# Kernel optimization log

Hardware: AMD Instinct MI355X
Metric: run time of the kernel (lower is better)

## Reference

```python
import jax, jax.numpy as jnp
import numpy as np

EPS = 1e-5
NUM_GROUPS = 32
HT_MIN = -2.0
HT_MAX = 2.0


def setup_inputs() -> dict:
    key = jax.random.key(0)
    k1, k2 = jax.random.split(key)
    B, Cin, Cout, H, W = 32, 256, 512, 56, 56
    x = jax.random.normal(k1, (B, Cin, H, W), dtype=jnp.float32)
    weight = jax.random.normal(k2, (Cout, Cin), dtype=jnp.float32)
    gamma = jnp.ones((Cout,), dtype=jnp.float32)
    beta = jnp.zeros((Cout,), dtype=jnp.float32)
    return {"x": x, "weight": weight, "gamma": gamma, "beta": beta}


def reference(x, weight, gamma, beta) -> jnp.ndarray:
    B, Cin, H, W = x.shape
    Cout = weight.shape[0]
    G = NUM_GROUPS
    # 1x1-conv style GEMM over channels (no bias in the original kernel call)
    y = jnp.einsum("oc,bchw->bohw", weight, x)  # [B, Cout, H, W]
    # GroupNorm: stats over (channels-in-group, H, W) per sample
    yg = y.reshape(B, G, Cout // G, H, W)
    mean = jnp.mean(yg, axis=(2, 3, 4), keepdims=True)
    var = jnp.var(yg, axis=(2, 3, 4), keepdims=True)
    yn = ((yg - mean) * jax.lax.rsqrt(var + EPS)).reshape(B, Cout, H, W)
    yn = yn * gamma[None, :, None, None] + beta[None, :, None, None]
    # HardTanh clamp
    return jnp.clip(yn, HT_MIN, HT_MAX)
```

## Files before the change

kernel.cpp:

```cpp
#include <hip/hip_runtime.h>


#define HW    3136
#define CIN   256
#define COUT  512
#define BATCH 32
#define NG    32
#define CPG   16
#define EPS   1e-5f

typedef _Float16 f16x8 __attribute__((ext_vector_type(8)));
typedef float    f32x4 __attribute__((ext_vector_type(4)));
typedef unsigned int u32;

__device__ __forceinline__ void gload16(const void* g, void* l) {
  __builtin_amdgcn_global_load_lds(
      (const u32 __attribute__((address_space(1)))*)g,
      (u32 __attribute__((address_space(3)))*)l, 16, 0, 0);
}

__global__ __launch_bounds__(256) void k0_transpose(
    const float* __restrict__ x, const float* __restrict__ w,
    _Float16* __restrict__ xT, _Float16* __restrict__ wf)
{
  __shared__ float T[64 * 65];
  const int bid = blockIdx.x;
  const int t   = threadIdx.x;
  const int b   = bid / 196;
  const int r   = bid % 196;
  const int st  = r >> 2;
  const int ct  = r & 3;
  const int s0  = st * 64, c0 = ct * 64;

  const float* xb = x + ((size_t)b * CIN + c0) * HW + s0;
#pragma unroll
  for (int rr = 0; rr < 4; ++rr) {
    const int c_loc = (t >> 4) + rr * 16;
    const int s4    = (t & 15) * 4;
    const float4 v  = *(const float4*)(xb + (size_t)c_loc * HW + s4);
    T[(s4 + 0) * 65 + c_loc] = v.x;
    T[(s4 + 1) * 65 + c_loc] = v.y;
    T[(s4 + 2) * 65 + c_loc] = v.z;
    T[(s4 + 3) * 65 + c_loc] = v.w;
  }
  __syncthreads();
#pragma unroll
  for (int p = 0; p < 2; ++p) {
    const int s_loc = p * 32 + (t >> 3);
    const int cg    = (t & 7) * 8;
    f16x8 o;
#pragma unroll
    for (int j = 0; j < 8; ++j) o[j] = (_Float16)T[s_loc * 65 + cg + j];
    *(f16x8*)(xT + ((size_t)b * HW + s0 + s_loc) * CIN + c0 + cg) = o;
  }
  if (bid < (COUT * CIN) / 256) wf[bid * 256 + t] = (_Float16)w[bid * 256 + t];
}

__global__ __launch_bounds__(256) void k_gemm(
    const _Float16* __restrict__ xT, const _Float16* __restrict__ wf,
    float2* __restrict__ stats, _Float16* __restrict__ y)
{
  __shared__ __align__(16) _Float16 As[2 * 128 * 32];
  __shared__ __align__(16) _Float16 Bs[2 * 128 * 32];

  const int bid  = blockIdx.x;
  const int tile = (bid & 7) * 400 + (bid >> 3);
  const int mt   = tile & 3;
  const int q2   = tile >> 2;
  const int nt   = q2 % 25;
  const int b    = q2 / 25;
  const int s0   = (nt == 24) ? (HW - 128) : nt * 128;

  const int t    = threadIdx.x;
  const int lane = t & 63;
  const int wid  = t >> 6;
  const int wy   = wid >> 1, wx = wid & 1;

  const int r_st = t >> 2;
  const int ch   = (t & 3) ^ ((r_st >> 1) & 3);

  const _Float16* xb = xT + (size_t)b * HW * CIN;
  const _Float16* gA0 = wf + (size_t)(mt * 128 + r_st) * CIN + ch * 8;
  const _Float16* gA1 = gA0 + (size_t)64 * CIN;
  const _Float16* gB0 = xb + (size_t)(s0 + r_st) * CIN + ch * 8;
  const _Float16* gB1 = gB0 + (size_t)64 * CIN;

  f32x4 acc[4][4] = {};

#define STAGE(bufi, kt_)                                                  \
  do {                                                                    \
    gload16(gA0 + (kt_) * 32, As + (bufi) * 4096 + t * 8);                \
    gload16(gA1 + (kt_) * 32, As + (bufi) * 4096 + 2048 + t * 8);         \
    gload16(gB0 + (kt_) * 32, Bs + (bufi) * 4096 + t * 8);                \
    gload16(gB1 + (kt_) * 32, Bs + (bufi) * 4096 + 2048 + t * 8);         \
  } while (0)

  STAGE(0, 0);
  __syncthreads();

  const int c = lane >> 4;
#pragma unroll
  for (int kt = 0; kt < 8; ++kt) {
    const int cur = kt & 1;
    if (kt < 7) STAGE(cur ^ 1, kt + 1);

    f16x8 af[4], bfr[4];
#pragma unroll
    for (int mi = 0; mi < 4; ++mi) {
      const int m = wy * 64 + mi * 16 + (lane & 15);
      af[mi] = *(const f16x8*)(As + cur * 4096 + m * 32 +
                               ((c ^ ((m >> 1) & 3)) * 8));
    }
#pragma unroll
    for (int ni = 0; ni < 4; ++ni) {
      const int n = wx * 64 + ni * 16 + (lane & 15);
      bfr[ni] = *(const f16x8*)(Bs + cur * 4096 + n * 32 +
                                ((c ^ ((n >> 1) & 3)) * 8));
    }
#pragma unroll
    for (int mi = 0; mi < 4; ++mi)
#pragma unroll
      for (int ni = 0; ni < 4; ++ni)
        acc[mi][ni] = __builtin_amdgcn_mfma_f32_16x16x32_f16(
            af[mi], bfr[ni], acc[mi][ni], 0, 0, 0);

    __syncthreads();
  }
#undef STAGE

  const int slo  = (nt == 24) ? 3072 : 0;
  const int colb = s0 + wx * 64 + (lane & 15);
#pragma unroll
  for (int mi = 0; mi < 4; ++mi) {
    float s1 = 0.f, s2 = 0.f;
#pragma unroll
    for (int ni = 0; ni < 4; ++ni) {
      if (colb + ni * 16 >= slo) {
#pragma unroll
        for (int rr = 0; rr < 4; ++rr) {
          const float v = acc[mi][ni][rr];
          s1 += v; s2 += v * v;
        }
      }
    }
#pragma unroll
    for (int off = 32; off > 0; off >>= 1) {
      s1 += __shfl_down(s1, off, 64);
      s2 += __shfl_down(s2, off, 64);
    }
    if (lane == 0) {
      const int g = mt * 8 + wy * 4 + mi;
      stats[((b * NG + g) * 25 + nt) * 2 + wx] = make_float2(s1, s2);
    }
    const int row0 = mt * 128 + wy * 64 + mi * 16 + ((lane >> 4) << 2);
#pragma unroll
    for (int rr = 0; rr < 4; ++rr) {
      _Float16* yrow = y + ((size_t)b * COUT + row0 + rr) * HW + colb;
#pragma unroll
      for (int ni = 0; ni < 4; ++ni)
        if (colb + ni * 16 >= slo) yrow[ni * 16] = (_Float16)acc[mi][ni][rr];
    }
  }
}

__global__ __launch_bounds__(256) void k_finalize(
    const float2* __restrict__ stats, const float* __restrict__ gamma,
    const float* __restrict__ beta, float* __restrict__ ss)
{
  const int i = blockIdx.x * 256 + threadIdx.x;
  if (i < BATCH * COUT) {
    const int b  = i >> 9;
    const int co = i & (COUT - 1);
    const int g  = co >> 4;
    const float2* sp = stats + (size_t)(b * NG + g) * 50;
    float s1 = 0.f, s2 = 0.f;
#pragma unroll 10
    for (int j = 0; j < 50; ++j) { s1 += sp[j].x; s2 += sp[j].y; }
    const float cnt  = (float)(CPG * HW);
    const float mean = s1 / cnt;
    const float var  = s2 / cnt - mean * mean;
    const float rsig = rsqrtf(var + EPS);
    const float sc   = rsig * gamma[co];
    ss[i * 2 + 0] = sc;
    ss[i * 2 + 1] = beta[co] - mean * sc;
  }
}

__global__ __launch_bounds__(256) void k_norm(
    const _Float16* __restrict__ y, const float* __restrict__ ss,
    float* __restrict__ out)
{
  const u32 u   = blockIdx.x * 256 + threadIdx.x;
  const u32 row = u / (HW / 8);
  const u32 sp  = (u - row * (HW / 8)) * 8;
  const float sc = ss[row * 2 + 0];
  const float sh = ss[row * 2 + 1];
  const f16x8 v = *(const f16x8*)(y + (size_t)row * HW + sp);
  f32x4 o0, o1;
  o0[0] = fminf(fmaxf((float)v[0] * sc + sh, -2.0f), 2.0f);
  o0[1] = fminf(fmaxf((float)v[1] * sc + sh, -2.0f), 2.0f);
  o0[2] = fminf(fmaxf((float)v[2] * sc + sh, -2.0f), 2.0f);
  o0[3] = fminf(fmaxf((float)v[3] * sc + sh, -2.0f), 2.0f);
  o1[0] = fminf(fmaxf((float)v[4] * sc + sh, -2.0f), 2.0f);
  o1[1] = fminf(fmaxf((float)v[5] * sc + sh, -2.0f), 2.0f);
  o1[2] = fminf(fmaxf((float)v[6] * sc + sh, -2.0f), 2.0f);
  o1[3] = fminf(fmaxf((float)v[7] * sc + sh, -2.0f), 2.0f);
  float* op = out + (size_t)row * HW + sp;
  __builtin_nontemporal_store(o0, (f32x4*)(op));
  __builtin_nontemporal_store(o1, (f32x4*)(op + 4));
}

extern "C" void kernel_launch(void* const* d_in, const int* in_sizes, int n_in,
                              void* d_out, int out_size, void* d_ws, size_t ws_size,
                              hipStream_t stream)
{
  const float* x     = (const float*)d_in[0];
  const float* w     = (const float*)d_in[1];
  const float* gamma = (const float*)d_in[2];
  const float* beta  = (const float*)d_in[3];
  float* out = (float*)d_out;

  const size_t xT_bytes = (size_t)BATCH * HW * CIN * 2;
  const size_t wf_bytes = (size_t)COUT * CIN * 2;
  const size_t st_bytes = (size_t)BATCH * NG * 50 * 8;
  const size_t ss_bytes = (size_t)BATCH * COUT * 2 * 4;
  const size_t y_bytes  = (size_t)BATCH * COUT * HW * 2;

  char* ws = (char*)d_ws;
  _Float16* xT = (_Float16*)ws;
  _Float16* wf = (_Float16*)(ws + xT_bytes);
  float2* stats = (float2*)(ws + xT_bytes + wf_bytes);
  float* ss    = (float*)(ws + xT_bytes + wf_bytes + st_bytes);
  _Float16* y  = (_Float16*)(ws + xT_bytes + wf_bytes + st_bytes + ss_bytes);

  if (ws_size < xT_bytes + wf_bytes + st_bytes + ss_bytes + y_bytes) return;

  k0_transpose<<<dim3(BATCH * 196), dim3(256), 0, stream>>>(x, w, xT, wf);
  k_gemm<<<dim3(BATCH * 100), dim3(256), 0, stream>>>(xT, wf, stats, y);
  k_finalize<<<dim3(BATCH * COUT / 256), dim3(256), 0, stream>>>(stats, gamma, beta, ss);
  k_norm<<<dim3(BATCH * COUT * HW / 8 / 256), dim3(256), 0, stream>>>(y, ss, out);
}
```

Measured before the change: 377.9 us.

## Recompute GEMM in a second pass to fuse normalization and drop fp16 intermediate

```diff
diff --git a/kernel.cpp b/kernel.cpp
--- a/kernel.cpp
+++ b/kernel.cpp
@@ -56,22 +56,13 @@
   if (bid < (COUT * CIN) / 256) wf[bid * 256 + t] = (_Float16)w[bid * 256 + t];
 }
 
-__global__ __launch_bounds__(256) void k_gemm(
+__device__ __forceinline__ void gemm_tile(
     const _Float16* __restrict__ xT, const _Float16* __restrict__ wf,
-    float2* __restrict__ stats, _Float16* __restrict__ y)
+    int b, int mt, int s0, int t, f32x4 (&acc)[4][4])
 {
   __shared__ __align__(16) _Float16 As[2 * 128 * 32];
   __shared__ __align__(16) _Float16 Bs[2 * 128 * 32];
 
-  const int bid  = blockIdx.x;
-  const int tile = (bid & 7) * 400 + (bid >> 3);
-  const int mt   = tile & 3;
-  const int q2   = tile >> 2;
-  const int nt   = q2 % 25;
-  const int b    = q2 / 25;
-  const int s0   = (nt == 24) ? (HW - 128) : nt * 128;
-
-  const int t    = threadIdx.x;
   const int lane = t & 63;
   const int wid  = t >> 6;
   const int wy   = wid >> 1, wx = wid & 1;
@@ -79,13 +70,11 @@
   const int r_st = t >> 2;
   const int ch   = (t & 3) ^ ((r_st >> 1) & 3);
 
-  const _Float16* xb = xT + (size_t)b * HW * CIN;
+  const _Float16* xb  = xT + (size_t)b * HW * CIN;
   const _Float16* gA0 = wf + (size_t)(mt * 128 + r_st) * CIN + ch * 8;
   const _Float16* gA1 = gA0 + (size_t)64 * CIN;
   const _Float16* gB0 = xb + (size_t)(s0 + r_st) * CIN + ch * 8;
   const _Float16* gB1 = gB0 + (size_t)64 * CIN;
-
-  f32x4 acc[4][4] = {};
 
 #define STAGE(bufi, kt_)                                                  \
   do {                                                                    \
@@ -127,6 +116,33 @@
     __syncthreads();
   }
 #undef STAGE
+}
+
+__device__ __forceinline__ void decode_tile(int bid, int& mt, int& nt,
+                                            int& b, int& s0)
+{
+  const int tile = (bid & 7) * 400 + (bid >> 3);
+  mt = tile & 3;
+  const int q2 = tile >> 2;
+  nt = q2 % 25;
+  b  = q2 / 25;
+  s0 = (nt == 24) ? (HW - 128) : nt * 128;
+}
+
+__global__ __launch_bounds__(256) void k_gemm_stats(
+    const _Float16* __restrict__ xT, const _Float16* __restrict__ wf,
+    float2* __restrict__ stats)
+{
+  int mt, nt, b, s0;
+  decode_tile(blockIdx.x, mt, nt, b, s0);
+
+  const int t    = threadIdx.x;
+  const int lane = t & 63;
+  const int wid  = t >> 6;
+  const int wy   = wid >> 1, wx = wid & 1;
+
+  f32x4 acc[4][4] = {};
+  gemm_tile(xT, wf, b, mt, s0, t, acc);
 
   const int slo  = (nt == 24) ? 3072 : 0;
   const int colb = s0 + wx * 64 + (lane & 15);
@@ -151,14 +167,6 @@
     if (lane == 0) {
       const int g = mt * 8 + wy * 4 + mi;
       stats[((b * NG + g) * 25 + nt) * 2 + wx] = make_float2(s1, s2);
-    }
-    const int row0 = mt * 128 + wy * 64 + mi * 16 + ((lane >> 4) << 2);
-#pragma unroll
-    for (int rr = 0; rr < 4; ++rr) {
-      _Float16* yrow = y + ((size_t)b * COUT + row0 + rr) * HW + colb;
-#pragma unroll
-      for (int ni = 0; ni < 4; ++ni)
-        if (colb + ni * 16 >= slo) yrow[ni * 16] = (_Float16)acc[mi][ni][rr];
     }
   }
 }
@@ -186,28 +194,40 @@
   }
 }
 
-__global__ __launch_bounds__(256) void k_norm(
-    const _Float16* __restrict__ y, const float* __restrict__ ss,
-    float* __restrict__ out)
-{
-  const u32 u   = blockIdx.x * 256 + threadIdx.x;
-  const u32 row = u / (HW / 8);
-  const u32 sp  = (u - row * (HW / 8)) * 8;
-  const float sc = ss[row * 2 + 0];
-  const float sh = ss[row * 2 + 1];
-  const f16x8 v = *(const f16x8*)(y + (size_t)row * HW + sp);
-  f32x4 o0, o1;
-  o0[0] = fminf(fmaxf((float)v[0] * sc + sh, -2.0f), 2.0f);
-  o0[1] = fminf(fmaxf((float)v[1] * sc + sh, -2.0f), 2.0f);
-  o0[2] = fminf(fmaxf((float)v[2] * sc + sh, -2.0f), 2.0f);
-  o0[3] = fminf(fmaxf((float)v[3] * sc + sh, -2.0f), 2.0f);
-  o1[0] = fminf(fmaxf((float)v[4] * sc + sh, -2.0f), 2.0f);
-  o1[1] = fminf(fmaxf((float)v[5] * sc + sh, -2.0f), 2.0f);
-  o1[2] = fminf(fmaxf((float)v[6] * sc + sh, -2.0f), 2.0f);
-  o1[3] = fminf(fmaxf((float)v[7] * sc + sh, -2.0f), 2.0f);
-  float* op = out + (size_t)row * HW + sp;
-  __builtin_nontemporal_store(o0, (f32x4*)(op));
-  __builtin_nontemporal_store(o1, (f32x4*)(op + 4));
+__global__ __launch_bounds__(256) void k_gemm_out(
+    const _Float16* __restrict__ xT, const _Float16* __restrict__ wf,
+    const float* __restrict__ ss, float* __restrict__ out)
+{
+  int mt, nt, b, s0;
+  decode_tile(blockIdx.x, mt, nt, b, s0);
+
+  const int t    = threadIdx.x;
+  const int lane = t & 63;
+  const int wid  = t >> 6;
+  const int wy   = wid >> 1, wx = wid & 1;
+
+  f32x4 acc[4][4] = {};
+  gemm_tile(xT, wf, b, mt, s0, t, acc);
+
+  const int slo  = (nt == 24) ? 3072 : 0;
+  const int colb = s0 + wx * 64 + (lane & 15);
+#pragma unroll
+  for (int mi = 0; mi < 4; ++mi) {
+    const int row0 = mt * 128 + wy * 64 + mi * 16 + ((lane >> 4) << 2);
+#pragma unroll
+    for (int rr = 0; rr < 4; ++rr) {
+      const int row = row0 + rr;
+      const float2 sv = *(const float2*)(ss + (size_t)(b * COUT + row) * 2);
+      float* orow = out + ((size_t)b * COUT + row) * HW + colb;
+#pragma unroll
+      for (int ni = 0; ni < 4; ++ni) {
+        if (colb + ni * 16 >= slo) {
+          const float v = acc[mi][ni][rr] * sv.x + sv.y;
+          orow[ni * 16] = fminf(fmaxf(v, -2.0f), 2.0f);
+        }
+      }
+    }
+  }
 }
 
 extern "C" void kernel_launch(void* const* d_in, const int* in_sizes, int n_in,
@@ -224,19 +244,17 @@
   const size_t wf_bytes = (size_t)COUT * CIN * 2;
   const size_t st_bytes = (size_t)BATCH * NG * 50 * 8;
   const size_t ss_bytes = (size_t)BATCH * COUT * 2 * 4;
-  const size_t y_bytes  = (size_t)BATCH * COUT * HW * 2;
 
   char* ws = (char*)d_ws;
-  _Float16* xT = (_Float16*)ws;
-  _Float16* wf = (_Float16*)(ws + xT_bytes);
-  float2* stats = (float2*)(ws + xT_bytes + wf_bytes);
-  float* ss    = (float*)(ws + xT_bytes + wf_bytes + st_bytes);
-  _Float16* y  = (_Float16*)(ws + xT_bytes + wf_bytes + st_bytes + ss_bytes);
-
-  if (ws_size < xT_bytes + wf_bytes + st_bytes + ss_bytes + y_bytes) return;
+  _Float16* xT  = (_Float16*)ws;
+  _Float16* wf  = (_Float16*)(ws + xT_bytes);
+  float2*  stats = (float2*)(ws + xT_bytes + wf_bytes);
+  float*   ss    = (float*)(ws + xT_bytes + wf_bytes + st_bytes);
+
+  if (ws_size < xT_bytes + wf_bytes + st_bytes + ss_bytes) return;
 
   k0_transpose<<<dim3(BATCH * 196), dim3(256), 0, stream>>>(x, w, xT, wf);
-  k_gemm<<<dim3(BATCH * 100), dim3(256), 0, stream>>>(xT, wf, stats, y);
+  k_gemm_stats<<<dim3(BATCH * 100), dim3(256), 0, stream>>>(xT, wf, stats);
   k_finalize<<<dim3(BATCH * COUT / 256), dim3(256), 0, stream>>>(stats, gamma, beta, ss);
-  k_norm<<<dim3(BATCH * COUT * HW / 8 / 256), dim3(256), 0, stream>>>(y, ss, out);
-}
+  k_gemm_out<<<dim3(BATCH * 100), dim3(256), 0, stream>>>(xT, wf, ss, out);
+}
```

Measured after the change: 387.2 us. 1.02x slower.
